# Performance work log

Hardware: AMD Instinct MI355X
Metric: run time of the kernel (lower is better)

Reference implementation:

```python
import jax, jax.numpy as jnp
import numpy as np

N, K, D = 32768, 8192, 64

def setup_inputs() -> dict:
    key = jax.random.key(0)
    kx, kc = jax.random.split(key)
    x = jax.random.normal(kx, (N, D), dtype=jnp.float32)
    codebook = jax.random.normal(kc, (K, D), dtype=jnp.float32)
    return {"x": x, "codebook": codebook}

def reference(x, codebook):
    # Faithful to: argmin(((codebook[None] - x[:, None])**2).sum(-1), -1)
    # Computed via the expanded squared distance to avoid the [N, K, D]
    # constant per row and does not affect argmin, but we include it so the
    # distance matrix matches the original math exactly.
    x_sq = jnp.sum(x * x, axis=-1, keepdims=True)          # [N, 1]
    c_sq = jnp.sum(codebook * codebook, axis=-1)           # [K]
    cross = jnp.einsum('nd,kd->nk', x, codebook)           # [N, K]
    dists = x_sq - 2.0 * cross + c_sq[None, :]             # [N, K]
    return jnp.argmin(dists, axis=-1)                      # [N] int32
```

## Files before the change

### kernel.cpp

```cpp
#include <hip/hip_runtime.h>
#include <math.h>


typedef __attribute__((ext_vector_type(8)))  _Float16 h8v;
typedef __attribute__((ext_vector_type(16))) float f16v;
typedef __attribute__((ext_vector_type(4)))  float f4v;

constexpr int NROWS = 32768;
constexpr int KC    = 8192;
constexpr int DD    = 64;
constexpr int TPB   = 256;
constexpr int BROWS = 64;
constexpr int BTILE = 64;
constexpr int NT    = KC / BTILE;
constexpr int TILE_HALFS = BTILE * DD * 2;
constexpr int BUF_HALFS  = TILE_HALFS + 512;

__device__ __forceinline__ void split2h(float v, _Float16& h1, _Float16& h2) {
  const float av = fabsf(v);
  _Float16 a = (_Float16)v;
  if (av < 6.1035156e-5f) a = (_Float16)0.f;
  h1 = a;
  h2 = (_Float16)((v - (float)a) * 4096.f);
}

__device__ __forceinline__ void gload_lds16(const void* g, void* l) {
  __builtin_amdgcn_global_load_lds(
      (const __attribute__((address_space(1))) void*)g,
      (__attribute__((address_space(3))) void*)l, 16, 0, 0);
}
__device__ __forceinline__ void gload_lds4(const void* g, void* l) {
  __builtin_amdgcn_global_load_lds(
      (const __attribute__((address_space(1))) void*)g,
      (__attribute__((address_space(3))) void*)l, 4, 0, 0);
}

__global__ void vq_pre_kernel(const float* __restrict__ cb,
                              _Float16* __restrict__ bSwz,
                              float* __restrict__ csq) {
  const int bid = blockIdx.x, tid = threadIdx.x;
  const int code = bid * TPB + tid;
  const float* cp = cb + (size_t)code * DD;
  float v[DD];
#pragma unroll
  for (int d = 0; d < DD; d += 4) {
    const float4 g = *(const float4*)(cp + d);
    v[d] = g.x; v[d + 1] = g.y; v[d + 2] = g.z; v[d + 3] = g.w;
  }
  float s = 0.f;
#pragma unroll
  for (int d = 0; d < DD; ++d) s = fmaf(v[d], v[d], s);
  csq[code] = s;
  _Float16 p1[DD], p2[DD];
#pragma unroll
  for (int d = 0; d < DD; ++d) split2h(v[d], p1[d], p2[d]);
  const int g = code >> 5, l = code & 31;
  _Float16* base = bSwz + (size_t)g * 4096;
#pragma unroll
  for (int p = 0; p < 2; ++p) {
    const _Float16* pl = p ? p2 : p1;
#pragma unroll
    for (int kc4 = 0; kc4 < 4; ++kc4)
#pragma unroll
      for (int h = 0; h < 2; ++h) {
        h8v wv;
#pragma unroll
        for (int j = 0; j < 8; ++j) wv[j] = pl[kc4 * 16 + h * 8 + j];
        *(h8v*)(base + (p * 4 + kc4) * 512 + (h * 32 + l) * 8) = wv;
      }
  }
}

#define TILE_BODY(T, BUFC, PFB, AA, AB, CS, CODE, PA, PB, PCS, PCODE, DOEPI, DOISSUE, WN) \
  {                                                                                       \
    _Float16* bp = ldsBf + (BUFC) * BUF_HALFS;                                            \
    h8v b0[4], b1[4];                                                                     \
    {                                                                                     \
      const _Float16* rb = bp + (ch * 8) * 512 + lane * 8;                                \
      _Pragma("unroll")                                                                   \
      for (int kc = 0; kc < 4; ++kc) {                                                    \
        b0[kc] = *(const h8v*)(rb + kc * 512);                                            \
        b1[kc] = *(const h8v*)(rb + (4 + kc) * 512);                                      \
      }                                                                                   \
    }                                                                                     \
    CS = ((const float*)(bp + TILE_HALFS))[w * 64 + wcode];                               \
    CODE = (unsigned)((T) * 64) + wcode;                                                  \
    if (DOISSUE) {                                                                        \
      const _Float16* gs = bSwz + (size_t)((T) + 2) * TILE_HALFS + (w * 4) * 512 + lane * 8; \
      _Float16* ld = ldsBf + (PFB) * BUF_HALFS;                                           \
      _Pragma("unroll")                                                                   \
      for (int j = 0; j < 4; ++j)                                                         \
        gload_lds16(gs + j * 512, ld + (w * 4 + j) * 512);                                \
      gload_lds4(csq_g + ((T) + 2) * 64 + lane, (float*)(ld + TILE_HALFS) + w * 64);      \
    }                                                                                     \
    AA = __builtin_amdgcn_mfma_f32_32x32x16_f16(afr[0][0], b0[0], Zacc, 0, 0, 0);         \
    AB = __builtin_amdgcn_mfma_f32_32x32x16_f16(afr[0][0], b1[0], Zacc, 0, 0, 0);         \
    _Pragma("unroll")                                                                     \
    for (int kc = 1; kc < 4; ++kc) {                                                      \
      AA = __builtin_amdgcn_mfma_f32_32x32x16_f16(afr[0][kc], b0[kc], AA, 0, 0, 0);       \
      AB = __builtin_amdgcn_mfma_f32_32x32x16_f16(afr[0][kc], b1[kc], AB, 0, 0, 0);       \
    }                                                                                     \
    _Pragma("unroll")                                                                     \
    for (int kc = 0; kc < 4; ++kc)                                                        \
      AB = __builtin_amdgcn_mfma_f32_32x32x16_f16(afr[1][kc], b0[kc], AB, 0, 0, 0);       \
    if (DOEPI) {                                                                          \
      _Pragma("unroll")                                                                   \
      for (int i = 0; i < 16; ++i) {                                                      \
        const float a_ = fmaf(PB[i], 2.44140625e-4f, PA[i]);                              \
        const float d_ = fmaf(-2.f, a_, xq[i]) + PCS;                                     \
        if (d_ < bestD[i]) { bestD[i] = d_; bestC[i] = PCODE; }                           \
      }                                                                                   \
    }                                                                                     \
    asm volatile("s_waitcnt vmcnt(" #WN ") lgkmcnt(0)\n\ts_barrier" ::: "memory");        \
  }

__global__ __launch_bounds__(TPB, 2)
void vq_mfma_kernel(const float* __restrict__ x, const _Float16* __restrict__ bSwz,
                    const float* __restrict__ csq_g, int* __restrict__ out) {
  __shared__ alignas(16) _Float16 ldsA[2][BROWS][DD];
  __shared__ alignas(16) _Float16 ldsBf[3 * BUF_HALFS];
  __shared__ alignas(16) float ldsXsq[BROWS];
  __shared__ unsigned long long ldsRed[BROWS][2];

  const int tid  = threadIdx.x;
  const int lane = tid & 63;
  const int w    = tid >> 6;
  const int s    = w & 1;
  const int ch   = w >> 1;
  const int half = lane >> 5;
  const int col  = lane & 31;
  const int wcode = ch * 32 + col;
  const int blockRow = blockIdx.x * BROWS;

#pragma unroll
  for (int tt = 0; tt < 2; ++tt) {
    const _Float16* gs = bSwz + (size_t)tt * TILE_HALFS + (w * 4) * 512 + lane * 8;
    _Float16* ld = ldsBf + tt * BUF_HALFS;
#pragma unroll
    for (int j = 0; j < 4; ++j)
      gload_lds16(gs + j * 512, ld + (w * 4 + j) * 512);
    gload_lds4(csq_g + tt * 64 + lane, (float*)(ld + TILE_HALFS) + w * 64);
  }
  {
    const int row = tid >> 2, dseg = (tid & 3) * 16;
    const float* xp = x + (size_t)(blockRow + row) * DD + dseg;
    float v[16];
#pragma unroll
    for (int d = 0; d < 16; d += 4) {
      const float4 g = *(const float4*)(xp + d);
      v[d] = g.x; v[d + 1] = g.y; v[d + 2] = g.z; v[d + 3] = g.w;
    }
    float p = 0.f;
#pragma unroll
    for (int e = 0; e < 16; ++e) p = fmaf(v[e], v[e], p);
    p += __shfl_xor(p, 1, 64);
    p += __shfl_xor(p, 2, 64);
    if ((tid & 3) == 0) ldsXsq[row] = p;
    _Float16 qa[16], qb[16];
#pragma unroll
    for (int e = 0; e < 16; ++e) split2h(v[e], qa[e], qb[e]);
#pragma unroll
    for (int h2 = 0; h2 < 2; ++h2) {
      h8v a, b;
#pragma unroll
      for (int j = 0; j < 8; ++j) { a[j] = qa[h2 * 8 + j]; b[j] = qb[h2 * 8 + j]; }
      *(h8v*)&ldsA[0][row][dseg + h2 * 8] = a;
      *(h8v*)&ldsA[1][row][dseg + h2 * 8] = b;
    }
  }
  __syncthreads();

  h8v afr[2][4];
#pragma unroll
  for (int p = 0; p < 2; ++p)
#pragma unroll
    for (int kc4 = 0; kc4 < 4; ++kc4)
      afr[p][kc4] = *(const h8v*)&ldsA[p][s * 32 + col][kc4 * 16 + half * 8];

  float xq[16];
  {
    const float* xb = &ldsXsq[s * 32 + 4 * half];
#pragma unroll
    for (int g8 = 0; g8 < 4; ++g8) {
      const f4v t4 = *(const f4v*)(xb + g8 * 8);
      xq[g8 * 4] = t4[0]; xq[g8 * 4 + 1] = t4[1];
      xq[g8 * 4 + 2] = t4[2]; xq[g8 * 4 + 3] = t4[3];
    }
  }

  float bestD[16];
  unsigned bestC[16];
#pragma unroll
  for (int i = 0; i < 16; ++i) { bestD[i] = INFINITY; bestC[i] = 0u; }

  const f16v Zacc = {0.f,0.f,0.f,0.f,0.f,0.f,0.f,0.f,0.f,0.f,0.f,0.f,0.f,0.f,0.f,0.f};
  f16v aA0 = Zacc, aB0 = Zacc, aA1 = Zacc, aB1 = Zacc;
  float cs0 = 0.f, cs1 = 0.f;
  unsigned code0 = 0u, code1 = 0u;

  TILE_BODY(0, 0, 2, aA0, aB0, cs0, code0, aA1, aB1, cs1, code1, false, true, 5);
  TILE_BODY(1, 1, 0, aA1, aB1, cs1, code1, aA0, aB0, cs0, code0, true,  true, 5);
  for (int t = 2; t < 122; t += 6) {
    TILE_BODY(t,     2, 1, aA0, aB0, cs0, code0, aA1, aB1, cs1, code1, true, true, 5);
    TILE_BODY(t + 1, 0, 2, aA1, aB1, cs1, code1, aA0, aB0, cs0, code0, true, true, 5);
    TILE_BODY(t + 2, 1, 0, aA0, aB0, cs0, code0, aA1, aB1, cs1, code1, true, true, 5);
    TILE_BODY(t + 3, 2, 1, aA1, aB1, cs1, code1, aA0, aB0, cs0, code0, true, true, 5);
    TILE_BODY(t + 4, 0, 2, aA0, aB0, cs0, code0, aA1, aB1, cs1, code1, true, true, 5);
    TILE_BODY(t + 5, 1, 0, aA1, aB1, cs1, code1, aA0, aB0, cs0, code0, true, true, 5);
  }
  TILE_BODY(122, 2, 1, aA0, aB0, cs0, code0, aA1, aB1, cs1, code1, true, true,  5);
  TILE_BODY(123, 0, 2, aA1, aB1, cs1, code1, aA0, aB0, cs0, code0, true, true,  5);
  TILE_BODY(124, 1, 0, aA0, aB0, cs0, code0, aA1, aB1, cs1, code1, true, true,  5);
  TILE_BODY(125, 2, 1, aA1, aB1, cs1, code1, aA0, aB0, cs0, code0, true, true,  5);
  TILE_BODY(126, 0, 2, aA0, aB0, cs0, code0, aA1, aB1, cs1, code1, true, false, 0);
  TILE_BODY(127, 1, 0, aA1, aB1, cs1, code1, aA0, aB0, cs0, code0, true, false, 0);
#pragma unroll
  for (int i = 0; i < 16; ++i) {
    const float a_ = fmaf(aB1[i], 2.44140625e-4f, aA1[i]);
    const float d_ = fmaf(-2.f, a_, xq[i]) + cs1;
    if (d_ < bestD[i]) { bestD[i] = d_; bestC[i] = code1; }
  }

  unsigned long long key[16];
#pragma unroll
  for (int i = 0; i < 16; ++i)
    key[i] = ((unsigned long long)__float_as_uint(bestD[i]) << 32) | bestC[i];
#pragma unroll
  for (int i = 0; i < 16; ++i) {
#pragma unroll
    for (int m = 1; m < 32; m <<= 1) {
      const unsigned long long o = __shfl_xor(key[i], m, 64);
      if (o < key[i]) key[i] = o;
    }
  }
  if (col == 0) {
#pragma unroll
    for (int i = 0; i < 16; ++i) {
      const int row = s * 32 + (i & 3) + 8 * (i >> 2) + 4 * half;
      ldsRed[row][ch] = key[i];
    }
  }
  __syncthreads();
  if (tid < BROWS) {
    const unsigned long long a = ldsRed[tid][0];
    const unsigned long long b = ldsRed[tid][1];
    out[blockRow + tid] = (int)(unsigned)((a < b ? a : b) & 0xFFFFFFFFull);
  }
}

extern "C" void kernel_launch(void* const* d_in, const int* in_sizes, int n_in,
                              void* d_out, int out_size, void* d_ws, size_t ws_size,
                              hipStream_t stream) {
  const float* x  = (const float*)d_in[0];
  const float* cb = (const float*)d_in[1];
  int* out = (int*)d_out;

  _Float16* bSwz = (_Float16*)d_ws;
  float* csq_g = (float*)((char*)d_ws + (size_t)KC * DD * 2 * 2);

  vq_pre_kernel<<<dim3(KC / TPB), dim3(TPB), 0, stream>>>(cb, bSwz, csq_g);
  vq_mfma_kernel<<<dim3(NROWS / BROWS), dim3(TPB), 0, stream>>>(
      x, bSwz, csq_g, out);
}
```

Before: 178.5 us.

## Double rows per block so each wave reuses codebook fragments across two row tiles

Raises the block's row count from 64 to 128. Each wave now handles 64 rows (two 32-row A tiles) against 32 codes, so every B fragment read from LDS feeds twice as many MFMAs and the codebook is streamed half as many times in total. The epilogue for the previous tile is split into two halves placed between MFMA groups to overlap it with compute. A is stored in LDS with an XOR-swizzled layout, and the preprocessing kernel is spread over four threads per code. Register use roughly doubles and occupancy drops to one block per CU, which risks less latency hiding.

```diff
diff --git a/kernel.cpp b/kernel.cpp
--- a/kernel.cpp
+++ b/kernel.cpp
@@ -10,7 +10,7 @@
 constexpr int KC    = 8192;
 constexpr int DD    = 64;
 constexpr int TPB   = 256;
-constexpr int BROWS = 64;
+constexpr int BROWS = 128;
 constexpr int BTILE = 64;
 constexpr int NT    = KC / BTILE;
 constexpr int TILE_HALFS = BTILE * DD * 2;
@@ -38,95 +38,112 @@
 __global__ void vq_pre_kernel(const float* __restrict__ cb,
                               _Float16* __restrict__ bSwz,
                               float* __restrict__ csq) {
-  const int bid = blockIdx.x, tid = threadIdx.x;
-  const int code = bid * TPB + tid;
-  const float* cp = cb + (size_t)code * DD;
-  float v[DD];
-#pragma unroll
-  for (int d = 0; d < DD; d += 4) {
+  const int gidx = blockIdx.x * TPB + threadIdx.x;
+  const int code = gidx >> 2;
+  const int kc4  = gidx & 3;
+  const float* cp = cb + (size_t)code * DD + kc4 * 16;
+  float v[16];
+#pragma unroll
+  for (int d = 0; d < 16; d += 4) {
     const float4 g = *(const float4*)(cp + d);
     v[d] = g.x; v[d + 1] = g.y; v[d + 2] = g.z; v[d + 3] = g.w;
   }
   float s = 0.f;
 #pragma unroll
-  for (int d = 0; d < DD; ++d) s = fmaf(v[d], v[d], s);
-  csq[code] = s;
-  _Float16 p1[DD], p2[DD];
-#pragma unroll
-  for (int d = 0; d < DD; ++d) split2h(v[d], p1[d], p2[d]);
+  for (int d = 0; d < 16; ++d) s = fmaf(v[d], v[d], s);
+  s += __shfl_xor(s, 1, 64);
+  s += __shfl_xor(s, 2, 64);
+  if (kc4 == 0) csq[code] = s;
+  _Float16 p1[16], p2[16];
+#pragma unroll
+  for (int d = 0; d < 16; ++d) split2h(v[d], p1[d], p2[d]);
   const int g = code >> 5, l = code & 31;
   _Float16* base = bSwz + (size_t)g * 4096;
 #pragma unroll
   for (int p = 0; p < 2; ++p) {
     const _Float16* pl = p ? p2 : p1;
 #pragma unroll
-    for (int kc4 = 0; kc4 < 4; ++kc4)
-#pragma unroll
-      for (int h = 0; h < 2; ++h) {
-        h8v wv;
-#pragma unroll
-        for (int j = 0; j < 8; ++j) wv[j] = pl[kc4 * 16 + h * 8 + j];
-        *(h8v*)(base + (p * 4 + kc4) * 512 + (h * 32 + l) * 8) = wv;
-      }
-  }
-}
-
-#define TILE_BODY(T, BUFC, PFB, AA, AB, CS, CODE, PA, PB, PCS, PCODE, DOEPI, DOISSUE, WN) \
-  {                                                                                       \
-    _Float16* bp = ldsBf + (BUFC) * BUF_HALFS;                                            \
-    h8v b0[4], b1[4];                                                                     \
-    {                                                                                     \
-      const _Float16* rb = bp + (ch * 8) * 512 + lane * 8;                                \
-      _Pragma("unroll")                                                                   \
-      for (int kc = 0; kc < 4; ++kc) {                                                    \
-        b0[kc] = *(const h8v*)(rb + kc * 512);                                            \
-        b1[kc] = *(const h8v*)(rb + (4 + kc) * 512);                                      \
-      }                                                                                   \
-    }                                                                                     \
-    CS = ((const float*)(bp + TILE_HALFS))[w * 64 + wcode];                               \
-    CODE = (unsigned)((T) * 64) + wcode;                                                  \
-    if (DOISSUE) {                                                                        \
+    for (int h = 0; h < 2; ++h) {
+      h8v wv;
+#pragma unroll
+      for (int j = 0; j < 8; ++j) wv[j] = pl[h * 8 + j];
+      *(h8v*)(base + (p * 4 + kc4) * 512 + (h * 32 + l) * 8) = wv;
+    }
+  }
+}
+
+#define TILE_BODY(T, BUFC, PFB, A0C, B0C, A1C, B1C, A0P, B0P, A1P, B1P, DOEPI, DOISSUE, WN) \
+  {                                                                                   \
+    const _Float16* bp = ldsBf + (BUFC) * BUF_HALFS;                                  \
+    h8v b0[4], b1[4];                                                                 \
+    {                                                                                 \
+      const _Float16* rb = bp + (ch * 8) * 512 + lane * 8;                            \
+      _Pragma("unroll")                                                               \
+      for (int kc = 0; kc < 4; ++kc) {                                                \
+        b0[kc] = *(const h8v*)(rb + kc * 512);                                        \
+        b1[kc] = *(const h8v*)(rb + (4 + kc) * 512);                                  \
+      }                                                                               \
+    }                                                                                 \
+    const float csC = ((const float*)(bp + TILE_HALFS))[w * 64 + wcode];              \
+    if (DOISSUE) {                                                                    \
       const _Float16* gs = bSwz + (size_t)((T) + 2) * TILE_HALFS + (w * 4) * 512 + lane * 8; \
-      _Float16* ld = ldsBf + (PFB) * BUF_HALFS;                                           \
-      _Pragma("unroll")                                                                   \
-      for (int j = 0; j < 4; ++j)                                                         \
-        gload_lds16(gs + j * 512, ld + (w * 4 + j) * 512);                                \
-      gload_lds4(csq_g + ((T) + 2) * 64 + lane, (float*)(ld + TILE_HALFS) + w * 64);      \
-    }                                                                                     \
-    AA = __builtin_amdgcn_mfma_f32_32x32x16_f16(afr[0][0], b0[0], Zacc, 0, 0, 0);         \
-    AB = __builtin_amdgcn_mfma_f32_32x32x16_f16(afr[0][0], b1[0], Zacc, 0, 0, 0);         \
-    _Pragma("unroll")                                                                     \
-    for (int kc = 1; kc < 4; ++kc) {                                                      \
-      AA = __builtin_amdgcn_mfma_f32_32x32x16_f16(afr[0][kc], b0[kc], AA, 0, 0, 0);       \
-      AB = __builtin_amdgcn_mfma_f32_32x32x16_f16(afr[0][kc], b1[kc], AB, 0, 0, 0);       \
-    }                                                                                     \
-    _Pragma("unroll")                                                                     \
-    for (int kc = 0; kc < 4; ++kc)                                                        \
-      AB = __builtin_amdgcn_mfma_f32_32x32x16_f16(afr[1][kc], b0[kc], AB, 0, 0, 0);       \
-    if (DOEPI) {                                                                          \
-      _Pragma("unroll")                                                                   \
-      for (int i = 0; i < 16; ++i) {                                                      \
-        const float a_ = fmaf(PB[i], 2.44140625e-4f, PA[i]);                              \
-        const float d_ = fmaf(-2.f, a_, xq[i]) + PCS;                                     \
-        if (d_ < bestD[i]) { bestD[i] = d_; bestC[i] = PCODE; }                           \
-      }                                                                                   \
-    }                                                                                     \
-    asm volatile("s_waitcnt vmcnt(" #WN ") lgkmcnt(0)\n\ts_barrier" ::: "memory");        \
-  }
-
-__global__ __launch_bounds__(TPB, 2)
+      _Float16* ld = ldsBf + (PFB) * BUF_HALFS;                                       \
+      _Pragma("unroll")                                                               \
+      for (int j = 0; j < 4; ++j)                                                     \
+        gload_lds16(gs + j * 512, ld + (w * 4 + j) * 512);                            \
+      gload_lds4(csq_g + ((T) + 2) * 64 + lane, (float*)(ld + TILE_HALFS) + w * 64);  \
+    }                                                                                 \
+    A0C = __builtin_amdgcn_mfma_f32_32x32x16_f16(afr[0][0][0], b0[0], Zacc, 0, 0, 0); \
+    A1C = __builtin_amdgcn_mfma_f32_32x32x16_f16(afr[1][0][0], b0[0], Zacc, 0, 0, 0); \
+    B0C = __builtin_amdgcn_mfma_f32_32x32x16_f16(afr[0][0][0], b1[0], Zacc, 0, 0, 0); \
+    B1C = __builtin_amdgcn_mfma_f32_32x32x16_f16(afr[1][0][0], b1[0], Zacc, 0, 0, 0); \
+    _Pragma("unroll")                                                                 \
+    for (int kc = 1; kc < 4; ++kc) {                                                  \
+      A0C = __builtin_amdgcn_mfma_f32_32x32x16_f16(afr[0][0][kc], b0[kc], A0C, 0, 0, 0); \
+      A1C = __builtin_amdgcn_mfma_f32_32x32x16_f16(afr[1][0][kc], b0[kc], A1C, 0, 0, 0); \
+      B0C = __builtin_amdgcn_mfma_f32_32x32x16_f16(afr[0][0][kc], b1[kc], B0C, 0, 0, 0); \
+      B1C = __builtin_amdgcn_mfma_f32_32x32x16_f16(afr[1][0][kc], b1[kc], B1C, 0, 0, 0); \
+    }                                                                                 \
+    if (DOEPI) {                                                                      \
+      const unsigned pcode = (unsigned)(((T) - 1) * 64) + wcode;                      \
+      _Pragma("unroll")                                                               \
+      for (int i = 0; i < 16; ++i) {                                                  \
+        const float a_ = fmaf(B0P[i], 2.44140625e-4f, A0P[i]);                        \
+        const float d_ = fmaf(-2.f, a_, xq[i]) + csP;                                 \
+        if (d_ < bestD[i]) { bestD[i] = d_; bestC[i] = pcode; }                       \
+      }                                                                               \
+    }                                                                                 \
+    _Pragma("unroll")                                                                 \
+    for (int kc = 0; kc < 4; ++kc) {                                                  \
+      B0C = __builtin_amdgcn_mfma_f32_32x32x16_f16(afr[0][1][kc], b0[kc], B0C, 0, 0, 0); \
+      B1C = __builtin_amdgcn_mfma_f32_32x32x16_f16(afr[1][1][kc], b0[kc], B1C, 0, 0, 0); \
+    }                                                                                 \
+    if (DOEPI) {                                                                      \
+      const unsigned pcode = (unsigned)(((T) - 1) * 64) + wcode;                      \
+      _Pragma("unroll")                                                               \
+      for (int i = 0; i < 16; ++i) {                                                  \
+        const float a_ = fmaf(B1P[i], 2.44140625e-4f, A1P[i]);                        \
+        const float d_ = fmaf(-2.f, a_, xq[16 + i]) + csP;                            \
+        if (d_ < bestD[16 + i]) { bestD[16 + i] = d_; bestC[16 + i] = pcode; }        \
+      }                                                                               \
+    }                                                                                 \
+    csP = csC;                                                                        \
+    asm volatile("s_waitcnt vmcnt(" #WN ") lgkmcnt(0)\n\ts_barrier" ::: "memory");    \
+  }
+
+__global__ __launch_bounds__(TPB, 1)
 void vq_mfma_kernel(const float* __restrict__ x, const _Float16* __restrict__ bSwz,
                     const float* __restrict__ csq_g, int* __restrict__ out) {
-  __shared__ alignas(16) _Float16 ldsA[2][BROWS][DD];
+  __shared__ alignas(16) _Float16 ldsAf[2 * BROWS * 8 * 8];
   __shared__ alignas(16) _Float16 ldsBf[3 * BUF_HALFS];
   __shared__ alignas(16) float ldsXsq[BROWS];
-  __shared__ unsigned long long ldsRed[BROWS][2];
+  __shared__ alignas(16) unsigned long long ldsRed[BROWS][2];
 
   const int tid  = threadIdx.x;
   const int lane = tid & 63;
   const int w    = tid >> 6;
-  const int s    = w & 1;
-  const int ch   = w >> 1;
+  const int ch   = w & 1;
+  const int rs   = w >> 1;
   const int half = lane >> 5;
   const int col  = lane & 31;
   const int wcode = ch * 32 + col;
@@ -142,91 +159,110 @@
     gload_lds4(csq_g + tt * 64 + lane, (float*)(ld + TILE_HALFS) + w * 64);
   }
   {
-    const int row = tid >> 2, dseg = (tid & 3) * 16;
-    const float* xp = x + (size_t)(blockRow + row) * DD + dseg;
-    float v[16];
-#pragma unroll
-    for (int d = 0; d < 16; d += 4) {
+    const int row = tid >> 1, off32 = (tid & 1) * 32;
+    const float* xp = x + (size_t)(blockRow + row) * DD + off32;
+    float v[32];
+#pragma unroll
+    for (int d = 0; d < 32; d += 4) {
       const float4 g = *(const float4*)(xp + d);
       v[d] = g.x; v[d + 1] = g.y; v[d + 2] = g.z; v[d + 3] = g.w;
     }
     float p = 0.f;
 #pragma unroll
-    for (int e = 0; e < 16; ++e) p = fmaf(v[e], v[e], p);
+    for (int e = 0; e < 32; ++e) p = fmaf(v[e], v[e], p);
     p += __shfl_xor(p, 1, 64);
-    p += __shfl_xor(p, 2, 64);
-    if ((tid & 3) == 0) ldsXsq[row] = p;
-    _Float16 qa[16], qb[16];
-#pragma unroll
-    for (int e = 0; e < 16; ++e) split2h(v[e], qa[e], qb[e]);
-#pragma unroll
-    for (int h2 = 0; h2 < 2; ++h2) {
-      h8v a, b;
-#pragma unroll
-      for (int j = 0; j < 8; ++j) { a[j] = qa[h2 * 8 + j]; b[j] = qb[h2 * 8 + j]; }
-      *(h8v*)&ldsA[0][row][dseg + h2 * 8] = a;
-      *(h8v*)&ldsA[1][row][dseg + h2 * 8] = b;
+    if ((tid & 1) == 0) ldsXsq[row] = p;
+    _Float16 qa[32], qb[32];
+#pragma unroll
+    for (int e = 0; e < 32; ++e) split2h(v[e], qa[e], qb[e]);
+#pragma unroll
+    for (int pidx = 0; pidx < 2; ++pidx) {
+      const _Float16* ql = pidx ? qb : qa;
+#pragma unroll
+      for (int h2 = 0; h2 < 4; ++h2) {
+        h8v wv;
+#pragma unroll
+        for (int j = 0; j < 8; ++j) wv[j] = ql[h2 * 8 + j];
+        const int slot = (tid & 1) * 4 + h2;
+        *(h8v*)&ldsAf[((pidx * BROWS + row) * 8 + (slot ^ (row & 7))) * 8] = wv;
+      }
     }
   }
   __syncthreads();
 
-  h8v afr[2][4];
-#pragma unroll
-  for (int p = 0; p < 2; ++p)
-#pragma unroll
-    for (int kc4 = 0; kc4 < 4; ++kc4)
-      afr[p][kc4] = *(const h8v*)&ldsA[p][s * 32 + col][kc4 * 16 + half * 8];
-
-  float xq[16];
-  {
-    const float* xb = &ldsXsq[s * 32 + 4 * half];
+  h8v afr[2][2][4];
+#pragma unroll
+  for (int q = 0; q < 2; ++q)
+#pragma unroll
+    for (int p = 0; p < 2; ++p)
+#pragma unroll
+      for (int kc = 0; kc < 4; ++kc) {
+        const int arow = rs * 64 + q * 32 + col;
+        const int slot = kc * 2 + half;
+        afr[q][p][kc] =
+            *(const h8v*)&ldsAf[((p * BROWS + arow) * 8 + (slot ^ (arow & 7))) * 8];
+      }
+
+  float xq[32];
+#pragma unroll
+  for (int q = 0; q < 2; ++q) {
+    const float* xb = &ldsXsq[rs * 64 + q * 32 + 4 * half];
 #pragma unroll
     for (int g8 = 0; g8 < 4; ++g8) {
       const f4v t4 = *(const f4v*)(xb + g8 * 8);
-      xq[g8 * 4] = t4[0]; xq[g8 * 4 + 1] = t4[1];
-      xq[g8 * 4 + 2] = t4[2]; xq[g8 * 4 + 3] = t4[3];
-    }
-  }
-
-  float bestD[16];
-  unsigned bestC[16];
-#pragma unroll
-  for (int i = 0; i < 16; ++i) { bestD[i] = INFINITY; bestC[i] = 0u; }
+      xq[q * 16 + g8 * 4]     = t4[0]; xq[q * 16 + g8 * 4 + 1] = t4[1];
+      xq[q * 16 + g8 * 4 + 2] = t4[2]; xq[q * 16 + g8 * 4 + 3] = t4[3];
+    }
+  }
+
+  float bestD[32];
+  unsigned bestC[32];
+#pragma unroll
+  for (int i = 0; i < 32; ++i) { bestD[i] = INFINITY; bestC[i] = 0u; }
 
   const f16v Zacc = {0.f,0.f,0.f,0.f,0.f,0.f,0.f,0.f,0.f,0.f,0.f,0.f,0.f,0.f,0.f,0.f};
-  f16v aA0 = Zacc, aB0 = Zacc, aA1 = Zacc, aB1 = Zacc;
-  float cs0 = 0.f, cs1 = 0.f;
-  unsigned code0 = 0u, code1 = 0u;
-
-  TILE_BODY(0, 0, 2, aA0, aB0, cs0, code0, aA1, aB1, cs1, code1, false, true, 5);
-  TILE_BODY(1, 1, 0, aA1, aB1, cs1, code1, aA0, aB0, cs0, code0, true,  true, 5);
+  f16v aA0e = Zacc, aB0e = Zacc, aA1e = Zacc, aB1e = Zacc;
+  f16v aA0o = Zacc, aB0o = Zacc, aA1o = Zacc, aB1o = Zacc;
+  float csP = 0.f;
+
+  TILE_BODY(0, 0, 2, aA0e, aB0e, aA1e, aB1e, aA0o, aB0o, aA1o, aB1o, false, true, 5);
+  TILE_BODY(1, 1, 0, aA0o, aB0o, aA1o, aB1o, aA0e, aB0e, aA1e, aB1e, true,  true, 5);
   for (int t = 2; t < 122; t += 6) {
-    TILE_BODY(t,     2, 1, aA0, aB0, cs0, code0, aA1, aB1, cs1, code1, true, true, 5);
-    TILE_BODY(t + 1, 0, 2, aA1, aB1, cs1, code1, aA0, aB0, cs0, code0, true, true, 5);
-    TILE_BODY(t + 2, 1, 0, aA0, aB0, cs0, code0, aA1, aB1, cs1, code1, true, true, 5);
-    TILE_BODY(t + 3, 2, 1, aA1, aB1, cs1, code1, aA0, aB0, cs0, code0, true, true, 5);
-    TILE_BODY(t + 4, 0, 2, aA0, aB0, cs0, code0, aA1, aB1, cs1, code1, true, true, 5);
-    TILE_BODY(t + 5, 1, 0, aA1, aB1, cs1, code1, aA0, aB0, cs0, code0, true, true, 5);
-  }
-  TILE_BODY(122, 2, 1, aA0, aB0, cs0, code0, aA1, aB1, cs1, code1, true, true,  5);
-  TILE_BODY(123, 0, 2, aA1, aB1, cs1, code1, aA0, aB0, cs0, code0, true, true,  5);
-  TILE_BODY(124, 1, 0, aA0, aB0, cs0, code0, aA1, aB1, cs1, code1, true, true,  5);
-  TILE_BODY(125, 2, 1, aA1, aB1, cs1, code1, aA0, aB0, cs0, code0, true, true,  5);
-  TILE_BODY(126, 0, 2, aA0, aB0, cs0, code0, aA1, aB1, cs1, code1, true, false, 0);
-  TILE_BODY(127, 1, 0, aA1, aB1, cs1, code1, aA0, aB0, cs0, code0, true, false, 0);
-#pragma unroll
-  for (int i = 0; i < 16; ++i) {
-    const float a_ = fmaf(aB1[i], 2.44140625e-4f, aA1[i]);
-    const float d_ = fmaf(-2.f, a_, xq[i]) + cs1;
-    if (d_ < bestD[i]) { bestD[i] = d_; bestC[i] = code1; }
-  }
-
-  unsigned long long key[16];
-#pragma unroll
-  for (int i = 0; i < 16; ++i)
+    TILE_BODY(t,     2, 1, aA0e, aB0e, aA1e, aB1e, aA0o, aB0o, aA1o, aB1o, true, true, 5);
+    TILE_BODY(t + 1, 0, 2, aA0o, aB0o, aA1o, aB1o, aA0e, aB0e, aA1e, aB1e, true, true, 5);
+    TILE_BODY(t + 2, 1, 0, aA0e, aB0e, aA1e, aB1e, aA0o, aB0o, aA1o, aB1o, true, true, 5);
+    TILE_BODY(t + 3, 2, 1, aA0o, aB0o, aA1o, aB1o, aA0e, aB0e, aA1e, aB1e, true, true, 5);
+    TILE_BODY(t + 4, 0, 2, aA0e, aB0e, aA1e, aB1e, aA0o, aB0o, aA1o, aB1o, true, true, 5);
+    TILE_BODY(t + 5, 1, 0, aA0o, aB0o, aA1o, aB1o, aA0e, aB0e, aA1e, aB1e, true, true, 5);
+  }
+  TILE_BODY(122, 2, 1, aA0e, aB0e, aA1e, aB1e, aA0o, aB0o, aA1o, aB1o, true, true,  5);
+  TILE_BODY(123, 0, 2, aA0o, aB0o, aA1o, aB1o, aA0e, aB0e, aA1e, aB1e, true, true,  5);
+  TILE_BODY(124, 1, 0, aA0e, aB0e, aA1e, aB1e, aA0o, aB0o, aA1o, aB1o, true, true,  5);
+  TILE_BODY(125, 2, 1, aA0o, aB0o, aA1o, aB1o, aA0e, aB0e, aA1e, aB1e, true, true,  5);
+  TILE_BODY(126, 0, 0, aA0e, aB0e, aA1e, aB1e, aA0o, aB0o, aA1o, aB1o, true, false, 0);
+  TILE_BODY(127, 1, 0, aA0o, aB0o, aA1o, aB1o, aA0e, aB0e, aA1e, aB1e, true, false, 0);
+  {
+    const unsigned code127 = (unsigned)(127 * 64) + wcode;
+#pragma unroll
+    for (int i = 0; i < 16; ++i) {
+      const float a_ = fmaf(aB0o[i], 2.44140625e-4f, aA0o[i]);
+      const float d_ = fmaf(-2.f, a_, xq[i]) + csP;
+      if (d_ < bestD[i]) { bestD[i] = d_; bestC[i] = code127; }
+    }
+#pragma unroll
+    for (int i = 0; i < 16; ++i) {
+      const float a_ = fmaf(aB1o[i], 2.44140625e-4f, aA1o[i]);
+      const float d_ = fmaf(-2.f, a_, xq[16 + i]) + csP;
+      if (d_ < bestD[16 + i]) { bestD[16 + i] = d_; bestC[16 + i] = code127; }
+    }
+  }
+
+  unsigned long long key[32];
+#pragma unroll
+  for (int i = 0; i < 32; ++i)
     key[i] = ((unsigned long long)__float_as_uint(bestD[i]) << 32) | bestC[i];
 #pragma unroll
-  for (int i = 0; i < 16; ++i) {
+  for (int i = 0; i < 32; ++i) {
 #pragma unroll
     for (int m = 1; m < 32; m <<= 1) {
       const unsigned long long o = __shfl_xor(key[i], m, 64);
@@ -235,8 +271,9 @@
   }
   if (col == 0) {
 #pragma unroll
-    for (int i = 0; i < 16; ++i) {
-      const int row = s * 32 + (i & 3) + 8 * (i >> 2) + 4 * half;
+    for (int i = 0; i < 32; ++i) {
+      const int ii = i & 15, q = i >> 4;
+      const int row = rs * 64 + q * 32 + (ii & 3) + 8 * (ii >> 2) + 4 * half;
       ldsRed[row][ch] = key[i];
     }
   }
@@ -258,7 +295,7 @@
   _Float16* bSwz = (_Float16*)d_ws;
   float* csq_g = (float*)((char*)d_ws + (size_t)KC * DD * 2 * 2);
 
-  vq_pre_kernel<<<dim3(KC / TPB), dim3(TPB), 0, stream>>>(cb, bSwz, csq_g);
+  vq_pre_kernel<<<dim3(KC * 4 / TPB), dim3(TPB), 0, stream>>>(cb, bSwz, csq_g);
   vq_mfma_kernel<<<dim3(NROWS / BROWS), dim3(TPB), 0, stream>>>(
       x, bSwz, csq_g, out);
 }
```

Result: no change. 176.8 us (-1.0%).
